# Optimization experiments

Hardware: AMD Instinct MI355X
Metric: run time of the kernel (lower is better)

The kernel has to match this reference:

```python
import jax, jax.numpy as jnp
import numpy as np

GAMMA = 1.0

def setup_inputs() -> dict:
    key = jax.random.key(0)
    kx, ky = jax.random.split(key)
    x = jax.random.normal(kx, (8192, 256), dtype=jnp.float32)
    y = jax.random.normal(ky, (8192, 256), dtype=jnp.float32)
    return {"x": x, "y": y}

def reference(x, y):
    # RBF kernel K[i,j] = exp(-gamma * ||x_i - y_j||^2)
    # materializing the O(N*M*D) broadcast difference tensor.
    x2 = jnp.sum(x * x, axis=-1)            # [N]
    y2 = jnp.sum(y * y, axis=-1)            # [M]
    xy = jnp.einsum('nd,md->nm', x, y)      # [N, M] GEMM
    dist2 = x2[:, None] + y2[None, :] - 2.0 * xy
    dist2 = jnp.maximum(dist2, 0.0)         # guard tiny negative round-off
    return jnp.exp(-GAMMA * dist2)
```

## Files before the change

kernel.cpp:

```cpp
#include <hip/hip_runtime.h>


#define M_DIM 8192
#define K_DIM 256
#define BM 64
#define BN 64

typedef __attribute__((ext_vector_type(4))) float float4v;
typedef __attribute__((ext_vector_type(4))) int   int4v;
typedef __attribute__((ext_vector_type(8))) int   int8v;

__global__ __launch_bounds__(256) void prep_kernel(
        const float* __restrict__ x, const float* __restrict__ y,
        unsigned char* __restrict__ xb, unsigned char* __restrict__ yb,
        float* __restrict__ x2, float* __restrict__ y2) {
    int row  = blockIdx.x * 4 + (threadIdx.x >> 6);
    int lane = threadIdx.x & 63;

    const float* src; unsigned char* dst; float* nrm; int r;
    if (row < M_DIM) { src = x; dst = xb; nrm = x2; r = row; }
    else             { src = y; dst = yb; nrm = y2; r = row - M_DIM; }

    const float4* s4 = (const float4*)(src + (size_t)r * K_DIM);
    float4 v = s4[lane];
    float ss = v.x * v.x + v.y * v.y + v.z * v.z + v.w * v.w;

    int packed = __builtin_amdgcn_cvt_pk_fp8_f32(v.x, v.y, 0, false);
    packed     = __builtin_amdgcn_cvt_pk_fp8_f32(v.z, v.w, packed, true);

    int u  = lane >> 2;
    int su = u ^ (r & 15);
    *(unsigned int*)(dst + (size_t)r * 256 + su * 16 + (lane & 3) * 4) =
        (unsigned int)packed;

    #pragma unroll
    for (int o = 32; o > 0; o >>= 1) ss += __shfl_down(ss, o);
    if (lane == 0) nrm[r] = ss;
}

__global__ __launch_bounds__(256, 4) void rbf_gemm(
        const unsigned char* __restrict__ xb, const unsigned char* __restrict__ yb,
        const float* __restrict__ x2, const float* __restrict__ y2,
        float* __restrict__ out) {
    __shared__ __align__(16) unsigned char smem[BM * 256 + BN * 256];
    unsigned char* As = smem;
    unsigned char* Bs = smem + BM * 256;

    const int tid  = threadIdx.x;
    const int wid  = tid >> 6;
    const int lane = tid & 63;
    const int wm   = wid >> 1;
    const int wn   = wid & 1;

    const int bid = blockIdx.x;
    const int xcd = bid & 7;
    const int lin = bid >> 3;
    const int ty  = (xcd << 4) + (lin >> 7);
    const int tx  = lin & 127;
    const int m0  = ty * BM;
    const int n0  = tx * BN;

    #pragma unroll
    for (int i = 0; i < 4; ++i) {
        const int ch = wid * 4 + i;
        __builtin_amdgcn_global_load_lds(
            (__attribute__((address_space(1))) void*)
                (xb + (size_t)(m0 + ch * 4) * 256 + lane * 16),
            (__attribute__((address_space(3))) void*)&As[ch * 1024],
            16, 0, 0);
    }
    #pragma unroll
    for (int i = 0; i < 4; ++i) {
        const int ch = wid * 4 + i;
        __builtin_amdgcn_global_load_lds(
            (__attribute__((address_space(1))) void*)
                (yb + (size_t)(n0 + ch * 4) * 256 + lane * 16),
            (__attribute__((address_space(3))) void*)&Bs[ch * 1024],
            16, 0, 0);
    }

    const int q = lane >> 4;
    const int c = lane & 15;
    float   x2s[2];
    float4v y2q[2];
    #pragma unroll
    for (int mt = 0; mt < 2; ++mt)
        x2s[mt] = x2[m0 + wm * 32 + mt * 16 + c];
    #pragma unroll
    for (int nt = 0; nt < 2; ++nt)
        y2q[nt] = *(const float4v*)&y2[n0 + wn * 32 + nt * 16 + q * 4];

    __syncthreads();

    const int fr = lane & 15;
    const int g  = lane >> 4;

    float4v acc[2][2] = {};

    #pragma unroll
    for (int ks = 0; ks < 2; ++ks) {
        const int p0 = 8 * ks + 2 * g;
        const int u0 = ((p0 ^ fr) << 4);
        const int u1 = (((p0 + 1) ^ fr) << 4);
        int8v a[2], b[2];
        #pragma unroll
        for (int mt = 0; mt < 2; ++mt) {
            const int rb = (wm * 32 + mt * 16 + fr) * 256;
            int4v lo = *(const int4v*)&As[rb + u0];
            int4v hi = *(const int4v*)&As[rb + u1];
            a[mt] = (int8v){lo.x, lo.y, lo.z, lo.w, hi.x, hi.y, hi.z, hi.w};
        }
        #pragma unroll
        for (int nt = 0; nt < 2; ++nt) {
            const int rb = (wn * 32 + nt * 16 + fr) * 256;
            int4v lo = *(const int4v*)&Bs[rb + u0];
            int4v hi = *(const int4v*)&Bs[rb + u1];
            b[nt] = (int8v){lo.x, lo.y, lo.z, lo.w, hi.x, hi.y, hi.z, hi.w};
        }
        #pragma unroll
        for (int mt = 0; mt < 2; ++mt)
            #pragma unroll
            for (int nt = 0; nt < 2; ++nt)
                acc[mt][nt] = __builtin_amdgcn_mfma_scale_f32_16x16x128_f8f6f4(
                    b[nt], a[mt], acc[mt][nt], 0, 0, 0, 0x7F, 0, 0x7F);
    }

    #pragma unroll
    for (int mt = 0; mt < 2; ++mt) {
        const size_t rowbase = (size_t)(m0 + wm * 32 + mt * 16 + c) * M_DIM;
        #pragma unroll
        for (int nt = 0; nt < 2; ++nt) {
            float dv[4];
            #pragma unroll
            for (int v = 0; v < 4; ++v) {
                float d = x2s[mt] + y2q[nt][v] - 2.0f * acc[mt][nt][v];
                dv[v] = fmaxf(d, 0.0f);
            }
            float4v r = {0.0f, 0.0f, 0.0f, 0.0f};
            bool anylt = (dv[0] < 105.0f) | (dv[1] < 105.0f) |
                         (dv[2] < 105.0f) | (dv[3] < 105.0f);
            if (__ballot(anylt) != 0ULL) {
                #pragma unroll
                for (int v = 0; v < 4; ++v)
                    r[v] = (dv[v] < 105.0f) ? __expf(-dv[v]) : 0.0f;
            }
            *(float4v*)&out[rowbase + n0 + wn * 32 + nt * 16 + q * 4] = r;
        }
    }
}

__global__ void rbf_naive(const float* __restrict__ x, const float* __restrict__ y,
                          float* __restrict__ out) {
    __shared__ float xs[16][17];
    __shared__ float ys[16][17];
    const int tx = threadIdx.x, ty = threadIdx.y;
    const int row = blockIdx.y * 16 + ty;
    const int col = blockIdx.x * 16 + tx;
    float acc = 0.0f;
    for (int k0 = 0; k0 < K_DIM; k0 += 16) {
        xs[ty][tx] = x[(size_t)row * K_DIM + k0 + tx];
        ys[ty][tx] = y[(size_t)(blockIdx.x * 16 + ty) * K_DIM + k0 + tx];
        __syncthreads();
        #pragma unroll
        for (int kk = 0; kk < 16; ++kk) {
            float d = xs[ty][kk] - ys[tx][kk];
            acc += d * d;
        }
        __syncthreads();
    }
    out[(size_t)row * M_DIM + col] = __expf(-acc);
}

extern "C" void kernel_launch(void* const* d_in, const int* in_sizes, int n_in,
                              void* d_out, int out_size, void* d_ws, size_t ws_size,
                              hipStream_t stream) {
    const float* x = (const float*)d_in[0];
    const float* y = (const float*)d_in[1];
    float* out = (float*)d_out;

    const size_t need = (size_t)2 * M_DIM * 256
                      + (size_t)2 * M_DIM * sizeof(float);
    if (ws_size >= need) {
        unsigned char* xb = (unsigned char*)d_ws;
        unsigned char* yb = xb + (size_t)M_DIM * 256;
        float* x2 = (float*)(yb + (size_t)M_DIM * 256);
        float* y2 = x2 + M_DIM;

        prep_kernel<<<dim3((2 * M_DIM) / 4), dim3(256), 0, stream>>>(x, y, xb, yb, x2, y2);
        rbf_gemm<<<dim3((M_DIM / BM) * (M_DIM / BN)), dim3(256), 0, stream>>>(xb, yb, x2, y2, out);
    } else {
        rbf_naive<<<dim3(M_DIM / 16, M_DIM / 16), dim3(16, 16), 0, stream>>>(x, y, out);
    }
}
```

Baseline: 285.4 us.

## Load FP8 MFMA operands directly from global into registers, skipping LDS staging

```diff
diff --git a/kernel.cpp b/kernel.cpp
--- a/kernel.cpp
+++ b/kernel.cpp
@@ -28,10 +28,7 @@
     int packed = __builtin_amdgcn_cvt_pk_fp8_f32(v.x, v.y, 0, false);
     packed     = __builtin_amdgcn_cvt_pk_fp8_f32(v.z, v.w, packed, true);
 
-    int u  = lane >> 2;
-    int su = u ^ (r & 15);
-    *(unsigned int*)(dst + (size_t)r * 256 + su * 16 + (lane & 3) * 4) =
-        (unsigned int)packed;
+    *(unsigned int*)(dst + (size_t)r * 256 + lane * 4) = (unsigned int)packed;
 
     #pragma unroll
     for (int o = 32; o > 0; o >>= 1) ss += __shfl_down(ss, o);
@@ -42,10 +39,6 @@
         const unsigned char* __restrict__ xb, const unsigned char* __restrict__ yb,
         const float* __restrict__ x2, const float* __restrict__ y2,
         float* __restrict__ out) {
-    __shared__ __align__(16) unsigned char smem[BM * 256 + BN * 256];
-    unsigned char* As = smem;
-    unsigned char* Bs = smem + BM * 256;
-
     const int tid  = threadIdx.x;
     const int wid  = tid >> 6;
     const int lane = tid & 63;
@@ -60,23 +53,24 @@
     const int m0  = ty * BM;
     const int n0  = tx * BN;
 
+    const int fr = lane & 15;
+    const int g  = lane >> 4;
+    const unsigned char* a0 = xb + (size_t)(m0 + wm * 32 + fr) * 256 + g * 32;
+    const unsigned char* a1 = a0 + 16 * 256;
+    const unsigned char* b0 = yb + (size_t)(n0 + wn * 32 + fr) * 256 + g * 32;
+    const unsigned char* b1 = b0 + 16 * 256;
+
+    int8v a[2][2], b[2][2];
     #pragma unroll
-    for (int i = 0; i < 4; ++i) {
-        const int ch = wid * 4 + i;
-        __builtin_amdgcn_global_load_lds(
-            (__attribute__((address_space(1))) void*)
-                (xb + (size_t)(m0 + ch * 4) * 256 + lane * 16),
-            (__attribute__((address_space(3))) void*)&As[ch * 1024],
-            16, 0, 0);
-    }
-    #pragma unroll
-    for (int i = 0; i < 4; ++i) {
-        const int ch = wid * 4 + i;
-        __builtin_amdgcn_global_load_lds(
-            (__attribute__((address_space(1))) void*)
-                (yb + (size_t)(n0 + ch * 4) * 256 + lane * 16),
-            (__attribute__((address_space(3))) void*)&Bs[ch * 1024],
-            16, 0, 0);
+    for (int ks = 0; ks < 2; ++ks) {
+        ((int4v*)&a[0][ks])[0] = *(const int4v*)(a0 + ks * 128);
+        ((int4v*)&a[0][ks])[1] = *(const int4v*)(a0 + ks * 128 + 16);
+        ((int4v*)&a[1][ks])[0] = *(const int4v*)(a1 + ks * 128);
+        ((int4v*)&a[1][ks])[1] = *(const int4v*)(a1 + ks * 128 + 16);
+        ((int4v*)&b[0][ks])[0] = *(const int4v*)(b0 + ks * 128);
+        ((int4v*)&b[0][ks])[1] = *(const int4v*)(b0 + ks * 128 + 16);
+        ((int4v*)&b[1][ks])[0] = *(const int4v*)(b1 + ks * 128);
+        ((int4v*)&b[1][ks])[1] = *(const int4v*)(b1 + ks * 128 + 16);
     }
 
     const int q = lane >> 4;
@@ -90,40 +84,15 @@
     for (int nt = 0; nt < 2; ++nt)
         y2q[nt] = *(const float4v*)&y2[n0 + wn * 32 + nt * 16 + q * 4];
 
-    __syncthreads();
-
-    const int fr = lane & 15;
-    const int g  = lane >> 4;
-
     float4v acc[2][2] = {};
-
     #pragma unroll
-    for (int ks = 0; ks < 2; ++ks) {
-        const int p0 = 8 * ks + 2 * g;
-        const int u0 = ((p0 ^ fr) << 4);
-        const int u1 = (((p0 + 1) ^ fr) << 4);
-        int8v a[2], b[2];
-        #pragma unroll
-        for (int mt = 0; mt < 2; ++mt) {
-            const int rb = (wm * 32 + mt * 16 + fr) * 256;
-            int4v lo = *(const int4v*)&As[rb + u0];
-            int4v hi = *(const int4v*)&As[rb + u1];
-            a[mt] = (int8v){lo.x, lo.y, lo.z, lo.w, hi.x, hi.y, hi.z, hi.w};
-        }
-        #pragma unroll
-        for (int nt = 0; nt < 2; ++nt) {
-            const int rb = (wn * 32 + nt * 16 + fr) * 256;
-            int4v lo = *(const int4v*)&Bs[rb + u0];
-            int4v hi = *(const int4v*)&Bs[rb + u1];
-            b[nt] = (int8v){lo.x, lo.y, lo.z, lo.w, hi.x, hi.y, hi.z, hi.w};
-        }
+    for (int ks = 0; ks < 2; ++ks)
         #pragma unroll
         for (int mt = 0; mt < 2; ++mt)
             #pragma unroll
             for (int nt = 0; nt < 2; ++nt)
                 acc[mt][nt] = __builtin_amdgcn_mfma_scale_f32_16x16x128_f8f6f4(
-                    b[nt], a[mt], acc[mt][nt], 0, 0, 0, 0x7F, 0, 0x7F);
-    }
+                    b[nt][ks], a[mt][ks], acc[mt][nt], 0, 0, 0, 0x7F, 0, 0x7F);
 
     #pragma unroll
     for (int mt = 0; mt < 2; ++mt) {
@@ -144,7 +113,8 @@
                 for (int v = 0; v < 4; ++v)
                     r[v] = (dv[v] < 105.0f) ? __expf(-dv[v]) : 0.0f;
             }
-            *(float4v*)&out[rowbase + n0 + wn * 32 + nt * 16 + q * 4] = r;
+            __builtin_nontemporal_store(
+                r, (float4v*)&out[rowbase + n0 + wn * 32 + nt * 16 + q * 4]);
         }
     }
 }
```

Result: slower. 358.6 us (+25.6%).

## Loop each block over 16 N-tiles with register-resident A and double-buffered B

Applied to the files above, without the earlier changes.

```diff
diff --git a/kernel.cpp b/kernel.cpp
--- a/kernel.cpp
+++ b/kernel.cpp
@@ -5,6 +5,7 @@
 #define K_DIM 256
 #define BM 64
 #define BN 64
+#define NT 16
 
 typedef __attribute__((ext_vector_type(4))) float float4v;
 typedef __attribute__((ext_vector_type(4))) int   int4v;
@@ -38,13 +39,11 @@
     if (lane == 0) nrm[r] = ss;
 }
 
-__global__ __launch_bounds__(256, 4) void rbf_gemm(
+__global__ __launch_bounds__(256, 3) void rbf_gemm(
         const unsigned char* __restrict__ xb, const unsigned char* __restrict__ yb,
         const float* __restrict__ x2, const float* __restrict__ y2,
         float* __restrict__ out) {
-    __shared__ __align__(16) unsigned char smem[BM * 256 + BN * 256];
-    unsigned char* As = smem;
-    unsigned char* Bs = smem + BM * 256;
+    __shared__ __align__(16) unsigned char Bs[2][BN * 256];
 
     const int tid  = threadIdx.x;
     const int wid  = tid >> 6;
@@ -55,96 +54,124 @@
     const int bid = blockIdx.x;
     const int xcd = bid & 7;
     const int lin = bid >> 3;
-    const int ty  = (xcd << 4) + (lin >> 7);
-    const int tx  = lin & 127;
+    const int ty  = (xcd << 4) + (lin >> 3);
+    const int tx0 = (lin & 7) << 4;
     const int m0  = ty * BM;
-    const int n0  = tx * BN;
+
+    const int fr = lane & 15;
+    const int g  = lane >> 4;
+    const int q  = lane >> 4;
+    const int c  = lane & 15;
 
     #pragma unroll
     for (int i = 0; i < 4; ++i) {
         const int ch = wid * 4 + i;
         __builtin_amdgcn_global_load_lds(
             (__attribute__((address_space(1))) void*)
-                (xb + (size_t)(m0 + ch * 4) * 256 + lane * 16),
-            (__attribute__((address_space(3))) void*)&As[ch * 1024],
+                (yb + (size_t)(tx0 * BN + ch * 4) * 256 + lane * 16),
+            (__attribute__((address_space(3))) void*)&Bs[0][ch * 1024],
             16, 0, 0);
     }
-    #pragma unroll
-    for (int i = 0; i < 4; ++i) {
-        const int ch = wid * 4 + i;
-        __builtin_amdgcn_global_load_lds(
-            (__attribute__((address_space(1))) void*)
-                (yb + (size_t)(n0 + ch * 4) * 256 + lane * 16),
-            (__attribute__((address_space(3))) void*)&Bs[ch * 1024],
-            16, 0, 0);
-    }
-
-    const int q = lane >> 4;
-    const int c = lane & 15;
-    float   x2s[2];
-    float4v y2q[2];
+
+    int8v a[2][2];
+    #pragma unroll
+    for (int mt = 0; mt < 2; ++mt) {
+        const unsigned char* ar =
+            xb + (size_t)(m0 + wm * 32 + mt * 16 + fr) * 256;
+        #pragma unroll
+        for (int ks = 0; ks < 2; ++ks) {
+            const int p0 = 8 * ks + 2 * g;
+            int4v lo = *(const int4v*)(ar + ((p0 ^ fr) << 4));
+            int4v hi = *(const int4v*)(ar + (((p0 + 1) ^ fr) << 4));
+            a[mt][ks] = (int8v){lo.x, lo.y, lo.z, lo.w,
+                                hi.x, hi.y, hi.z, hi.w};
+        }
+    }
+    float x2s[2];
     #pragma unroll
     for (int mt = 0; mt < 2; ++mt)
         x2s[mt] = x2[m0 + wm * 32 + mt * 16 + c];
-    #pragma unroll
-    for (int nt = 0; nt < 2; ++nt)
-        y2q[nt] = *(const float4v*)&y2[n0 + wn * 32 + nt * 16 + q * 4];
 
     __syncthreads();
 
-    const int fr = lane & 15;
-    const int g  = lane >> 4;
-
-    float4v acc[2][2] = {};
-
-    #pragma unroll
-    for (int ks = 0; ks < 2; ++ks) {
-        const int p0 = 8 * ks + 2 * g;
-        const int u0 = ((p0 ^ fr) << 4);
-        const int u1 = (((p0 + 1) ^ fr) << 4);
-        int8v a[2], b[2];
+    int cur = 0;
+    for (int t = 0; t < NT; ++t) {
+        const int n0 = (tx0 + t) * BN;
+
+        if (t + 1 < NT) {
+            const int n1 = (tx0 + t + 1) * BN;
+            #pragma unroll
+            for (int i = 0; i < 4; ++i) {
+                const int ch = wid * 4 + i;
+                __builtin_amdgcn_global_load_lds(
+                    (__attribute__((address_space(1))) void*)
+                        (yb + (size_t)(n1 + ch * 4) * 256 + lane * 16),
+                    (__attribute__((address_space(3))) void*)
+                        &Bs[cur ^ 1][ch * 1024],
+                    16, 0, 0);
+            }
+        }
+
+        float4v y2q[2];
+        #pragma unroll
+        for (int nt = 0; nt < 2; ++nt)
+            y2q[nt] = *(const float4v*)&y2[n0 + wn * 32 + nt * 16 + q * 4];
+
+        int8v b[2][2];
+        #pragma unroll
+        for (int ks = 0; ks < 2; ++ks) {
+            const int p0 = 8 * ks + 2 * g;
+            const int u0 = ((p0 ^ fr) << 4);
+            const int u1 = (((p0 + 1) ^ fr) << 4);
+            #pragma unroll
+            for (int nt = 0; nt < 2; ++nt) {
+                const int rb = (wn * 32 + nt * 16 + fr) * 256;
+                int4v lo = *(const int4v*)&Bs[cur][rb + u0];
+                int4v hi = *(const int4v*)&Bs[cur][rb + u1];
+                b[nt][ks] = (int8v){lo.x, lo.y, lo.z, lo.w,
+                                    hi.x, hi.y, hi.z, hi.w};
+            }
+        }
+
+        float4v acc[2][2] = {};
+        #pragma unroll
+        for (int ks = 0; ks < 2; ++ks)
+            #pragma unroll
+            for (int mt = 0; mt < 2; ++mt)
+                #pragma unroll
+                for (int nt = 0; nt < 2; ++nt)
+                    acc[mt][nt] =
+                        __builtin_amdgcn_mfma_scale_f32_16x16x128_f8f6f4(
+                            b[nt][ks], a[mt][ks], acc[mt][nt],
+                            0, 0, 0, 0x7F, 0, 0x7F);
+
         #pragma unroll
         for (int mt = 0; mt < 2; ++mt) {
-            const int rb = (wm * 32 + mt * 16 + fr) * 256;
-            int4v lo = *(const int4v*)&As[rb + u0];
-            int4v hi = *(const int4v*)&As[rb + u1];
-            a[mt] = (int8v){lo.x, lo.y, lo.z, lo.w, hi.x, hi.y, hi.z, hi.w};
-        }
-        #pragma unroll
-        for (int nt = 0; nt < 2; ++nt) {
-            const int rb = (wn * 32 + nt * 16 + fr) * 256;
-            int4v lo = *(const int4v*)&Bs[rb + u0];
-            int4v hi = *(const int4v*)&Bs[rb + u1];
-            b[nt] = (int8v){lo.x, lo.y, lo.z, lo.w, hi.x, hi.y, hi.z, hi.w};
-        }
-        #pragma unroll
-        for (int mt = 0; mt < 2; ++mt)
-            #pragma unroll
-            for (int nt = 0; nt < 2; ++nt)
-                acc[mt][nt] = __builtin_amdgcn_mfma_scale_f32_16x16x128_f8f6f4(
-                    b[nt], a[mt], acc[mt][nt], 0, 0, 0, 0x7F, 0, 0x7F);
-    }
-
-    #pragma unroll
-    for (int mt = 0; mt < 2; ++mt) {
-        const size_t rowbase = (size_t)(m0 + wm * 32 + mt * 16 + c) * M_DIM;
-        #pragma unroll
-        for (int nt = 0; nt < 2; ++nt) {
-            float dv[4];
-            #pragma unroll
-            for (int v = 0; v < 4; ++v) {
-                float d = x2s[mt] + y2q[nt][v] - 2.0f * acc[mt][nt][v];
-                dv[v] = fmaxf(d, 0.0f);
+            const size_t rowbase =
+                (size_t)(m0 + wm * 32 + mt * 16 + c) * M_DIM;
+            #pragma unroll
+            for (int nt = 0; nt < 2; ++nt) {
+                float dv[4];
+                #pragma unroll
+                for (int v = 0; v < 4; ++v) {
+                    float d = x2s[mt] + y2q[nt][v] - 2.0f * acc[mt][nt][v];
+                    dv[v] = fmaxf(d, 0.0f);
+                }
+                float4v r = {0.0f, 0.0f, 0.0f, 0.0f};
+                bool anylt = (dv[0] < 105.0f) | (dv[1] < 105.0f) |
+                             (dv[2] < 105.0f) | (dv[3] < 105.0f);
+                if (__ballot(anylt) != 0ULL) {
+                    #pragma unroll
+                    for (int v = 0; v < 4; ++v)
+                        r[v] = (dv[v] < 105.0f) ? __expf(-dv[v]) : 0.0f;
+                }
+                *(float4v*)&out[rowbase + n0 + wn * 32 + nt * 16 + q * 4] = r;
             }
-            float4v r = {0.0f, 0.0f, 0.0f, 0.0f};
-            bool anylt = (dv[0] < 105.0f) | (dv[1] < 105.0f) |
-                         (dv[2] < 105.0f) | (dv[3] < 105.0f);
-            if (__ballot(anylt) != 0ULL) {
-                #pragma unroll
-                for (int v = 0; v < 4; ++v)
-                    r[v] = (dv[v] < 105.0f) ? __expf(-dv[v]) : 0.0f;
-            }
-            *(float4v*)&out[rowbase + n0 + wn * 32 + nt * 16 + q * 4] = r;
+        }
+
+        if (t + 1 < NT) {
+            asm volatile("s_waitcnt vmcnt(4)\n\ts_barrier" ::: "memory");
+            cur ^= 1;
         }
     }
 }
@@ -187,7 +214,7 @@
         float* y2 = x2 + M_DIM;
 
         prep_kernel<<<dim3((2 * M_DIM) / 4), dim3(256), 0, stream>>>(x, y, xb, yb, x2, y2);
-        rbf_gemm<<<dim3((M_DIM / BM) * (M_DIM / BN)), dim3(256), 0, stream>>>(xb, yb, x2, y2, out);
+        rbf_gemm<<<dim3((M_DIM / BM) * (M_DIM / BN) / NT), dim3(256), 0, stream>>>(xb, yb, x2, y2, out);
     } else {
         rbf_naive<<<dim3(M_DIM / 16, M_DIM / 16), dim3(16, 16), 0, stream>>>(x, y, out);
     }
```

Result: slower. 294.7 us (+3.2%).
